# Kernel tuning notes

Hardware: AMD Instinct MI355X
Metric: run time of the kernel (lower is better)

The kernel has to match this reference:

```python
import jax, jax.numpy as jnp
import numpy as np


def _idxct_last(x):
    """IDCT-like transform along the last axis (DREAMPlace idxct):
        y_u = sum_{k=0}^{N-1} x_k * cos(pi * k * (u + 0.5) / N)
    computed via the Makhoul FFT trick: phase-twiddle + length-N IFFT + even/odd reorder.
    """
    N = x.shape[-1]
    k = jnp.arange(N)
    # twiddle: exp(i*pi*k/(2N))  (this is what dct_cpp/dct_cuda precompute as expk)
    phase = jnp.exp(1j * jnp.pi * k.astype(jnp.float32) / (2.0 * N)).astype(jnp.complex64)
    z = x.astype(jnp.complex64) * phase
    # f_n = sum_k z_k exp(+i 2pi k n / N)  == N * ifft(z)
    v = jnp.real(jnp.fft.ifft(z, axis=-1)) * N
    half = (N + 1) // 2
    # de-interleave: y[2i] = v[i], y[2i+1] = v[N-1-i]
    y = jnp.zeros_like(x)
    y = y.at[..., 0::2].set(v[..., :half].astype(x.dtype))
    y = y.at[..., 1::2].set(jnp.flip(v[..., half:], axis=-1).astype(x.dtype))
    return y


def idcct2_math(x):
    """2D inverse discrete cosine-cosine transform (separable):
        y_{u,v} = sum_{p,q} x_{p,q} cos(pi p (u+0.5)/M) cos(pi q (v+0.5)/N)
    equivalent to idxct(idxct(x)^T)^T.
    """
    y = _idxct_last(x)                      # transform along last dim (N)
    y = _idxct_last(jnp.swapaxes(y, -1, -2))  # transform along first dim (M)
    return jnp.swapaxes(y, -1, -2)


def setup_inputs() -> dict:
    key = jax.random.key(0)
    M, N = 4096, 4096
    x = jax.random.normal(key, (M, N), dtype=jnp.float32)
    return {"x": x}


def reference(x):
    return idcct2_math(x)
```

## Files before the change

kernel.cpp:

```cpp
#include <hip/hip_runtime.h>
#include <hip/hip_bf16.h>

typedef unsigned short u16;
typedef u16 us4 __attribute__((ext_vector_type(4)));
typedef u16 us8 __attribute__((ext_vector_type(8)));
typedef __bf16 bf16x8 __attribute__((ext_vector_type(8)));
typedef float f32x4 __attribute__((ext_vector_type(4)));

#define NDIM 4096
#define HDIM 2048

__device__ __forceinline__ u16 bfbits(float f) {
    __hip_bfloat16 h = __float2bfloat16(f);
    return __builtin_bit_cast(u16, h);
}
__device__ __forceinline__ float bf2f(u16 b) {
    return __builtin_bit_cast(float, ((unsigned)b) << 16);
}

__device__ __forceinline__ void gload_lds16(const u16* g, u16* l) {
    __builtin_amdgcn_global_load_lds((__attribute__((address_space(1))) void*)g,
                                     (__attribute__((address_space(3))) void*)l,
                                     16, 0, 0);
}

__global__ __launch_bounds__(256) void k_prep(u16* __restrict__ Ce, u16* __restrict__ Co,
                                              const float* __restrict__ X,
                                              u16* __restrict__ Xe, u16* __restrict__ Xo) {
    __shared__ float tile[64][65];
    if (blockIdx.x < 2048) {
        int idx = blockIdx.x * 256 + threadIdx.x;
        int u = idx >> 8;
        int k0 = (idx & 255) * 8;
        unsigned step = (unsigned)(2 * u + 1);
        us8 e, o;
#pragma unroll
        for (int i = 0; i < 8; ++i) {
            unsigned kk = (unsigned)(k0 + i);
            unsigned te = (2u * kk * step) & 16383u;
            unsigned to = ((2u * kk + 1u) * step) & 16383u;
            e[i] = bfbits(cosf((float)te * 3.8349519697141029e-4f));
            o[i] = bfbits(cosf((float)to * 3.8349519697141029e-4f));
        }
        *(us8*)&Ce[(size_t)idx * 8] = e;
        *(us8*)&Co[(size_t)idx * 8] = o;
    } else {
        int b  = blockIdx.x - 2048;
        int bx = (b & 63) * 64;
        int by = (b >> 6) * 64;
        int t  = threadIdx.x;
        int lr = t >> 4, lc = (t & 15) * 4;
#pragma unroll
        for (int r = 0; r < 64; r += 16) {
            float4 v = *(const float4*)&X[(size_t)(by + lr + r) * NDIM + bx + lc];
            tile[lr + r][lc + 0] = v.x;
            tile[lr + r][lc + 1] = v.y;
            tile[lr + r][lc + 2] = v.z;
            tile[lr + r][lc + 3] = v.w;
        }
        __syncthreads();
        int jl = t >> 2;
        int s8 = (t & 3) * 8;
        us8 e, o;
#pragma unroll
        for (int i = 0; i < 8; ++i) {
            e[i] = bfbits(tile[2 * (s8 + i)][jl]);
            o[i] = bfbits(tile[2 * (s8 + i) + 1][jl]);
        }
        size_t base = (size_t)(bx + jl) * HDIM + (by >> 1) + s8;
        *(us8*)&Xe[base] = e;
        *(us8*)&Xo[base] = o;
    }
}

__global__ __launch_bounds__(256) void k_bfly1(const u16* __restrict__ S,
                                               const u16* __restrict__ D,
                                               u16* __restrict__ We,
                                               u16* __restrict__ Wo) {
    int idx = blockIdx.x * 256 + threadIdx.x;
    int u  = idx >> 9;
    int j0 = (idx & 511) * 8;
    us8 s8 = *(const us8*)&S[(size_t)u * NDIM + j0];
    us8 d8 = *(const us8*)&D[(size_t)u * NDIM + j0];
    us4 et, ot, eb, ob;
#pragma unroll
    for (int i = 0; i < 4; ++i) {
        float se = bf2f(s8[2 * i]),     de = bf2f(d8[2 * i]);
        float so = bf2f(s8[2 * i + 1]), dd = bf2f(d8[2 * i + 1]);
        et[i] = bfbits(se + de);  eb[i] = bfbits(se - de);
        ot[i] = bfbits(so + dd);  ob[i] = bfbits(so - dd);
    }
    size_t ct = (size_t)u * HDIM + (j0 >> 1);
    size_t cb = (size_t)(NDIM - 1 - u) * HDIM + (j0 >> 1);
    *(us4*)&We[ct] = et;  *(us4*)&Wo[ct] = ot;
    *(us4*)&We[cb] = eb;  *(us4*)&Wo[cb] = ob;
}

__global__ __launch_bounds__(256) void k_bfly2(const u16* __restrict__ S2,
                                               const u16* __restrict__ D2,
                                               float* __restrict__ Y) {
    int idx = blockIdx.x * 256 + threadIdx.x;
    int i  = idx >> 8;
    int v0 = (idx & 255) * 8;
    us8 s8 = *(const us8*)&S2[(size_t)i * HDIM + v0];
    us8 d8 = *(const us8*)&D2[(size_t)i * HDIM + v0];
    float sum[8], dif[8];
#pragma unroll
    for (int t = 0; t < 8; ++t) {
        float s = bf2f(s8[t]), d = bf2f(d8[t]);
        sum[t] = s + d;  dif[t] = s - d;
    }
    f32x4 a0, a1, r0, r1;
#pragma unroll
    for (int w = 0; w < 4; ++w) {
        a0[w] = sum[w];  a1[w] = sum[w + 4];
        r0[w] = dif[7 - w];  r1[w] = dif[3 - w];
    }
    float* row = Y + (size_t)i * NDIM;
    *(f32x4*)&row[v0]        = a0;
    *(f32x4*)&row[v0 + 4]    = a1;
    *(f32x4*)&row[4088 - v0] = r0;
    *(f32x4*)&row[4092 - v0] = r1;
}

#define BAR() do { asm volatile("" ::: "memory"); __builtin_amdgcn_s_barrier(); \
                   asm volatile("" ::: "memory"); } while (0)
#define WAITV(N) asm volatile("s_waitcnt vmcnt(" #N ")" ::: "memory")
#define THROTTLE() asm volatile("s_waitcnt lgkmcnt(8)" ::: "memory")

template <int NTK, int LOG_NTN>
__global__ __launch_bounds__(512, 2) void gemm256h(const u16* __restrict__ A0,
                                                   const u16* __restrict__ A1,
                                                   const u16* __restrict__ B0,
                                                   const u16* __restrict__ B1,
                                                   u16* __restrict__ out) {
    constexpr int KD  = NTK * 64;
    constexpr int NTN = 1 << LOG_NTN;
    constexpr int LDC = NTN * 256;
    constexpr int MTILES = 128 >> LOG_NTN;

    __shared__ u16 As[2 * 256 * 64];
    __shared__ u16 Bs[2 * 256 * 64];

    const int tid  = threadIdx.x;
    const int wave = tid >> 6;
    const int lane = tid & 63;

    const int bid = blockIdx.x;
    const int swz = (bid & 7) * 32 + (bid >> 3);
    const int half = swz >> 7;
    const int r    = swz & 127;
    const int bm   = (r >> LOG_NTN) * 256;
    const int bn   = (r & (NTN - 1)) * 256;

    const u16* A = half ? A1 : A0;
    const u16* B = half ? B1 : B0;
    u16* Cp = out + (size_t)half * MTILES * 256 * LDC;

    const int wr = wave >> 2;
    const int wc = wave & 3;

    const int srow = lane >> 3;
    const int scol = ((lane & 7) ^ srow) << 3;

    const int fr   = lane & 15;
    const int hi   = lane >> 4;
    const int slot0 = ((hi)     ^ (lane & 7)) << 3;
    const int slot1 = ((hi + 4) ^ (lane & 7)) << 3;
    const int aRow = (wr * 128 + fr) * 64;
    const int bRow = (wc * 64 + fr) * 64;

    f32x4 acc[8][4] = {};
    bf16x8 aR[4][2], b01[2][2], b23[2][2];

#define STAGE_A(TK, H, BOFF)                                                     \
    do {                                                                         \
        const int _tk = (TK) & (NTK - 1);                                        \
        _Pragma("unroll")                                                        \
        for (int q = 0; q < 2; ++q) {                                            \
            const int seg  = wave * 2 + q;                                       \
            const int row0 = (H) * 64 + (seg & 7) * 8 + (seg >> 3) * 128;        \
            const u16* _g = A + (size_t)(bm + row0 + srow) * KD + _tk * 64 + scol; \
            gload_lds16(_g, As + (BOFF) + row0 * 64 + lane * 8);                 \
        }                                                                        \
    } while (0)

#define STAGE_B(TK, H, BOFF)                                                     \
    do {                                                                         \
        const int _tk = (TK) & (NTK - 1);                                        \
        _Pragma("unroll")                                                        \
        for (int q = 0; q < 2; ++q) {                                            \
            const int seg  = wave * 2 + q;                                       \
            const int row0 = (H) * 32 + (seg & 3) * 8 + (seg >> 2) * 64;         \
            const u16* _g = B + (size_t)(bn + row0 + srow) * KD + _tk * 64 + scol; \
            gload_lds16(_g, Bs + (BOFF) + row0 * 64 + lane * 8);                 \
        }                                                                        \
    } while (0)

#define LOAD_A(MB, BOFF)                                                        \
    _Pragma("unroll")                                                           \
    for (int mm = 0; mm < 4; ++mm) {                                            \
        aR[mm][0] = __builtin_bit_cast(bf16x8, *(const us8*)(As + (BOFF) + aRow + ((MB) + mm) * 1024 + slot0)); \
        aR[mm][1] = __builtin_bit_cast(bf16x8, *(const us8*)(As + (BOFF) + aRow + ((MB) + mm) * 1024 + slot1)); \
    }

#define LOAD_B(DST, NB, BOFF)                                                   \
    _Pragma("unroll")                                                           \
    for (int nn = 0; nn < 2; ++nn) {                                            \
        DST[nn][0] = __builtin_bit_cast(bf16x8, *(const us8*)(Bs + (BOFF) + bRow + ((NB) + nn) * 1024 + slot0)); \
        DST[nn][1] = __builtin_bit_cast(bf16x8, *(const us8*)(Bs + (BOFF) + bRow + ((NB) + nn) * 1024 + slot1)); \
    }

#define MFMA_Q(MB, NB, BREG)                                                    \
    do {                                                                        \
        __builtin_amdgcn_s_setprio(1);                                          \
        _Pragma("unroll")                                                       \
        for (int kk = 0; kk < 2; ++kk)                                          \
            _Pragma("unroll")                                                   \
            for (int mm = 0; mm < 4; ++mm)                                      \
                _Pragma("unroll")                                               \
                for (int nn = 0; nn < 2; ++nn)                                  \
                    acc[(MB)+mm][(NB)+nn] = __builtin_amdgcn_mfma_f32_16x16x32_bf16(aR[mm][kk], BREG[nn][kk], acc[(MB)+mm][(NB)+nn], 0, 0, 0); \
        __builtin_amdgcn_s_setprio(0);                                          \
    } while (0)

    STAGE_B(0, 0, 0);
    STAGE_A(0, 0, 0);
    STAGE_B(0, 1, 0);
    STAGE_A(0, 1, 0);
    STAGE_B(1, 0, 16384);
    STAGE_A(1, 0, 16384);
    STAGE_B(1, 1, 16384);
    WAITV(6);
    BAR();

    for (int t = 0; t < NTK; t += 2) {
        LOAD_A(0, 0);
        LOAD_B(b01, 0, 0);
        STAGE_A(t + 1, 1, 16384);
        THROTTLE();
        BAR();
        MFMA_Q(0, 0, b01);
        BAR();
        LOAD_B(b23, 2, 0);
        STAGE_B(t + 2, 0, 0);
        BAR();
        MFMA_Q(0, 2, b23);
        BAR();
        LOAD_A(4, 0);
        STAGE_A(t + 2, 0, 0);
        BAR();
        MFMA_Q(4, 2, b23);
        BAR();
        STAGE_B(t + 2, 1, 0);
        BAR();
        MFMA_Q(4, 0, b01);
        WAITV(6);
        BAR();
        LOAD_A(0, 16384);
        LOAD_B(b01, 0, 16384);
        STAGE_A(t + 2, 1, 0);
        THROTTLE();
        BAR();
        MFMA_Q(0, 0, b01);
        BAR();
        LOAD_B(b23, 2, 16384);
        STAGE_B(t + 3, 0, 16384);
        BAR();
        MFMA_Q(0, 2, b23);
        BAR();
        LOAD_A(4, 16384);
        STAGE_A(t + 3, 0, 16384);
        BAR();
        MFMA_Q(4, 2, b23);
        BAR();
        STAGE_B(t + 3, 1, 16384);
        BAR();
        MFMA_Q(4, 0, b01);
        WAITV(6);
        BAR();
    }

    asm volatile("s_waitcnt vmcnt(0)" ::: "memory");

    const int orow0 = wr * 128 + hi * 4;
    const int ocol0 = bn + wc * 64 + fr;
#pragma unroll
    for (int m = 0; m < 8; ++m)
#pragma unroll
        for (int n = 0; n < 4; ++n) {
            f32x4 v = acc[m][n];
#pragma unroll
            for (int rr = 0; rr < 4; ++rr) {
                size_t off = (size_t)(bm + orow0 + m * 16 + rr) * LDC + (ocol0 + n * 16);
                Cp[off] = bfbits(v[rr]);
            }
        }
#undef STAGE_A
#undef STAGE_B
#undef LOAD_A
#undef LOAD_B
#undef MFMA_Q
}

extern "C" void kernel_launch(void* const* d_in, const int* in_sizes, int n_in,
                              void* d_out, int out_size, void* d_ws, size_t ws_size,
                              hipStream_t stream) {
    const float* X = (const float*)d_in[0];
    float* Y = (float*)d_out;

    const size_t QM = (size_t)HDIM * HDIM;
    u16* Ce = (u16*)d_ws;
    u16* Co = Ce + QM;
    u16* Xe = Co + QM;
    u16* Xo = Xe + 2 * QM;
    u16* S  = Xo + 2 * QM;
    u16* D  = S + 2 * QM;
    u16* We = Xe;
    u16* Wo = Xo;
    u16* S2 = S;
    u16* D2 = D;

    k_prep<<<6144, 256, 0, stream>>>(Ce, Co, X, Xe, Xo);
    gemm256h<32, 4><<<256, 512, 0, stream>>>(Ce, Co, Xe, Xo, S);
    k_bfly1<<<4096, 256, 0, stream>>>(S, D, We, Wo);
    gemm256h<32, 3><<<256, 512, 0, stream>>>(We, Wo, Ce, Co, S2);
    k_bfly2<<<4096, 256, 0, stream>>>(S2, D2, Y);
}
```

Baseline: 170.9 us.

## Fuse second GEMM with final butterfly, writing fp32 output directly

Replaces the second half-GEMM plus the separate k_bfly2 kernel with a new gemmY kernel. It accumulates the even and odd products in two register accumulator sets, using a three-buffer LDS pipeline, and applies the sum/difference butterfly in the epilogue, writing fp32 Y directly. This removes the bf16 intermediate round trip through memory and one kernel launch. The epilogue's scalar strided fp32 stores, including the mirrored column writes, may coalesce poorly. The lgkmcnt throttle in the first GEMM is also removed.

After: 172.0 us. No clear change (+0.7%).

```diff
diff --git a/kernel.cpp b/kernel.cpp
--- a/kernel.cpp
+++ b/kernel.cpp
@@ -23,6 +23,10 @@
                                      (__attribute__((address_space(3))) void*)l,
                                      16, 0, 0);
 }
+
+#define BAR() do { asm volatile("" ::: "memory"); __builtin_amdgcn_s_barrier(); \
+                   asm volatile("" ::: "memory"); } while (0)
+#define WAITV(N) asm volatile("s_waitcnt vmcnt(" #N ")" ::: "memory")
 
 __global__ __launch_bounds__(256) void k_prep(u16* __restrict__ Ce, u16* __restrict__ Co,
                                               const float* __restrict__ X,
@@ -96,38 +100,6 @@
     *(us4*)&We[cb] = eb;  *(us4*)&Wo[cb] = ob;
 }
 
-__global__ __launch_bounds__(256) void k_bfly2(const u16* __restrict__ S2,
-                                               const u16* __restrict__ D2,
-                                               float* __restrict__ Y) {
-    int idx = blockIdx.x * 256 + threadIdx.x;
-    int i  = idx >> 8;
-    int v0 = (idx & 255) * 8;
-    us8 s8 = *(const us8*)&S2[(size_t)i * HDIM + v0];
-    us8 d8 = *(const us8*)&D2[(size_t)i * HDIM + v0];
-    float sum[8], dif[8];
-#pragma unroll
-    for (int t = 0; t < 8; ++t) {
-        float s = bf2f(s8[t]), d = bf2f(d8[t]);
-        sum[t] = s + d;  dif[t] = s - d;
-    }
-    f32x4 a0, a1, r0, r1;
-#pragma unroll
-    for (int w = 0; w < 4; ++w) {
-        a0[w] = sum[w];  a1[w] = sum[w + 4];
-        r0[w] = dif[7 - w];  r1[w] = dif[3 - w];
-    }
-    float* row = Y + (size_t)i * NDIM;
-    *(f32x4*)&row[v0]        = a0;
-    *(f32x4*)&row[v0 + 4]    = a1;
-    *(f32x4*)&row[4088 - v0] = r0;
-    *(f32x4*)&row[4092 - v0] = r1;
-}
-
-#define BAR() do { asm volatile("" ::: "memory"); __builtin_amdgcn_s_barrier(); \
-                   asm volatile("" ::: "memory"); } while (0)
-#define WAITV(N) asm volatile("s_waitcnt vmcnt(" #N ")" ::: "memory")
-#define THROTTLE() asm volatile("s_waitcnt lgkmcnt(8)" ::: "memory")
-
 template <int NTK, int LOG_NTN>
 __global__ __launch_bounds__(512, 2) void gemm256h(const u16* __restrict__ A0,
                                                    const u16* __restrict__ A1,
@@ -238,7 +210,6 @@
         LOAD_A(0, 0);
         LOAD_B(b01, 0, 0);
         STAGE_A(t + 1, 1, 16384);
-        THROTTLE();
         BAR();
         MFMA_Q(0, 0, b01);
         BAR();
@@ -260,7 +231,6 @@
         LOAD_A(0, 16384);
         LOAD_B(b01, 0, 16384);
         STAGE_A(t + 2, 1, 0);
-        THROTTLE();
         BAR();
         MFMA_Q(0, 0, b01);
         BAR();
@@ -303,6 +273,148 @@
 #undef MFMA_Q
 }
 
+__global__ __launch_bounds__(512, 2) void gemmY(const u16* __restrict__ We,
+                                                const u16* __restrict__ Wo,
+                                                const u16* __restrict__ Ce,
+                                                const u16* __restrict__ Co,
+                                                float* __restrict__ Y) {
+    constexpr int KD = 2048;
+    constexpr int BUF0 = 0, BUF1 = 24576, BUF2 = 49152;
+    __shared__ u16 LDS[3 * 24576];
+
+    const int tid  = threadIdx.x;
+    const int wave = tid >> 6;
+    const int lane = tid & 63;
+
+    const int bid = blockIdx.x;
+    const int swz = (bid & 7) * 32 + (bid >> 3);
+    const int bi  = (swz >> 4) * 256;
+    const int bv  = (swz & 15) * 128;
+
+    const int wr = wave >> 2;
+    const int wc = wave & 3;
+
+    const int srow = lane >> 3;
+    const int scol = ((lane & 7) ^ srow) << 3;
+
+    const int fr   = lane & 15;
+    const int hi   = lane >> 4;
+    const int slot0 = ((hi)     ^ (lane & 7)) << 3;
+    const int slot1 = ((hi + 4) ^ (lane & 7)) << 3;
+    const int aRow = (wr * 128 + fr) * 64;
+    const int bRow = (wc * 32 + fr) * 64;
+
+    f32x4 accS[8][2] = {}, accD[8][2] = {};
+    bf16x8 aR[4][2], bb[2][2];
+
+#define STAGE_AY(GP, TK, BUF)                                                   \
+    do {                                                                        \
+        _Pragma("unroll")                                                       \
+        for (int q = 0; q < 4; ++q) {                                           \
+            const int seg = wave * 4 + q;                                       \
+            const u16* _g = (GP) + (size_t)(bi + seg * 8 + srow) * KD + (TK) * 64 + scol; \
+            gload_lds16(_g, LDS + (BUF) + seg * 512 + lane * 8);                \
+        }                                                                       \
+    } while (0)
+
+#define STAGE_BY(GP, TK, BUF)                                                   \
+    do {                                                                        \
+        _Pragma("unroll")                                                       \
+        for (int q = 0; q < 2; ++q) {                                           \
+            const int seg = wave * 2 + q;                                       \
+            const u16* _g = (GP) + (size_t)(bv + seg * 8 + srow) * KD + (TK) * 64 + scol; \
+            gload_lds16(_g, LDS + (BUF) + 16384 + seg * 512 + lane * 8);        \
+        }                                                                       \
+    } while (0)
+
+#define LOAD_AY(MB, BUF)                                                        \
+    _Pragma("unroll")                                                           \
+    for (int mm = 0; mm < 4; ++mm) {                                            \
+        aR[mm][0] = __builtin_bit_cast(bf16x8, *(const us8*)(LDS + (BUF) + aRow + ((MB) + mm) * 1024 + slot0)); \
+        aR[mm][1] = __builtin_bit_cast(bf16x8, *(const us8*)(LDS + (BUF) + aRow + ((MB) + mm) * 1024 + slot1)); \
+    }
+
+#define LOAD_BY(BUF)                                                            \
+    _Pragma("unroll")                                                           \
+    for (int nn = 0; nn < 2; ++nn) {                                            \
+        bb[nn][0] = __builtin_bit_cast(bf16x8, *(const us8*)(LDS + (BUF) + 16384 + bRow + nn * 1024 + slot0)); \
+        bb[nn][1] = __builtin_bit_cast(bf16x8, *(const us8*)(LDS + (BUF) + 16384 + bRow + nn * 1024 + slot1)); \
+    }
+
+#define MFMA16(ACC, MB)                                                         \
+    do {                                                                        \
+        __builtin_amdgcn_s_setprio(1);                                          \
+        _Pragma("unroll")                                                       \
+        for (int kk = 0; kk < 2; ++kk)                                          \
+            _Pragma("unroll")                                                   \
+            for (int mm = 0; mm < 4; ++mm)                                      \
+                _Pragma("unroll")                                               \
+                for (int nn = 0; nn < 2; ++nn)                                  \
+                    ACC[(MB)+mm][nn] = __builtin_amdgcn_mfma_f32_16x16x32_bf16(aR[mm][kk], bb[nn][kk], ACC[(MB)+mm][nn], 0, 0, 0); \
+        __builtin_amdgcn_s_setprio(0);                                          \
+    } while (0)
+
+#define SUBTILE(ACC, BUF, BUFN, GA, GB, TKN)                                    \
+    do {                                                                        \
+        LOAD_AY(0, BUF);                                                        \
+        LOAD_BY(BUF);                                                           \
+        STAGE_AY(GA, TKN, BUFN);                                                \
+        BAR();                                                                  \
+        MFMA16(ACC, 0);                                                         \
+        BAR();                                                                  \
+        LOAD_AY(4, BUF);                                                        \
+        STAGE_BY(GB, TKN, BUFN);                                                \
+        BAR();                                                                  \
+        MFMA16(ACC, 4);                                                         \
+        WAITV(6);                                                               \
+        BAR();                                                                  \
+    } while (0)
+
+    STAGE_AY(We, 0, BUF0);
+    STAGE_BY(Ce, 0, BUF0);
+    STAGE_AY(Wo, 0, BUF1);
+    STAGE_BY(Co, 0, BUF1);
+    WAITV(6);
+    BAR();
+
+    for (int t = 0; t < 30; t += 3) {
+        SUBTILE(accS, BUF0, BUF2, We, Ce, (t + 1));
+        SUBTILE(accD, BUF1, BUF0, Wo, Co, (t + 1));
+        SUBTILE(accS, BUF2, BUF1, We, Ce, (t + 2));
+        SUBTILE(accD, BUF0, BUF2, Wo, Co, (t + 2));
+        SUBTILE(accS, BUF1, BUF0, We, Ce, (t + 3) & 31);
+        SUBTILE(accD, BUF2, BUF1, Wo, Co, (t + 3) & 31);
+    }
+    SUBTILE(accS, BUF0, BUF2, We, Ce, 31);
+    SUBTILE(accD, BUF1, BUF0, Wo, Co, 31);
+    SUBTILE(accS, BUF2, BUF1, We, Ce, 0);
+    SUBTILE(accD, BUF0, BUF2, Wo, Co, 0);
+
+    asm volatile("s_waitcnt vmcnt(0)" ::: "memory");
+
+    const int orow0 = bi + wr * 128 + hi * 4;
+    const int ocol0 = bv + wc * 32 + fr;
+#pragma unroll
+    for (int m = 0; m < 8; ++m)
+#pragma unroll
+        for (int n = 0; n < 2; ++n) {
+            f32x4 s = accS[m][n], d = accD[m][n];
+#pragma unroll
+            for (int rr = 0; rr < 4; ++rr) {
+                int row = orow0 + m * 16 + rr;
+                int vp  = ocol0 + n * 16;
+                Y[(size_t)row * NDIM + vp]            = s[rr] + d[rr];
+                Y[(size_t)row * NDIM + (NDIM - 1 - vp)] = s[rr] - d[rr];
+            }
+        }
+#undef STAGE_AY
+#undef STAGE_BY
+#undef LOAD_AY
+#undef LOAD_BY
+#undef MFMA16
+#undef SUBTILE
+}
+
 extern "C" void kernel_launch(void* const* d_in, const int* in_sizes, int n_in,
                               void* d_out, int out_size, void* d_ws, size_t ws_size,
                               hipStream_t stream) {
@@ -318,12 +430,9 @@
     u16* D  = S + 2 * QM;
     u16* We = Xe;
     u16* Wo = Xo;
-    u16* S2 = S;
-    u16* D2 = D;
 
     k_prep<<<6144, 256, 0, stream>>>(Ce, Co, X, Xe, Xo);
     gemm256h<32, 4><<<256, 512, 0, stream>>>(Ce, Co, Xe, Xo, S);
     k_bfly1<<<4096, 256, 0, stream>>>(S, D, We, Wo);
-    gemm256h<32, 3><<<256, 512, 0, stream>>>(We, Wo, Ce, Co, S2);
-    k_bfly2<<<4096, 256, 0, stream>>>(S2, D2, Y);
-}
+    gemmY<<<256, 512, 0, stream>>>(We, Wo, Ce, Co, Y);
+}
```
